# Performance work log

Measured on AMD Instinct MI355X. Metric: run time of the kernel, lower is better.

## Reference

```python
import jax, jax.numpy as jnp
import numpy as np

DIM = 1024
N_HEADS = 16
HEAD_DIM = DIM // N_HEADS
B, T = 4, 2048


def setup_inputs() -> dict:
    key = jax.random.key(0)
    k_x, k_cos, k_sin, k_wqkv, k_wout = jax.random.split(key, 5)
    x = jax.random.normal(k_x, (B, T, DIM), dtype=jnp.float32)
    # rotary tables indexed by position, half the head dim
    pos = jnp.arange(T, dtype=jnp.float32)[:, None]
    inv_freq = 1.0 / (10000.0 ** (jnp.arange(0, HEAD_DIM, 2, dtype=jnp.float32) / HEAD_DIM))
    ang = pos * inv_freq[None, :]  # [T, HEAD_DIM//2]
    cos = jnp.cos(ang)
    sin = jnp.sin(ang)
    mask = jnp.zeros((T, T), dtype=jnp.float32)
    Wqkv = jax.random.normal(k_wqkv, (3 * DIM, DIM), dtype=jnp.float32) * 0.02
    Wout = jax.random.normal(k_wout, (DIM, DIM), dtype=jnp.float32) * 0.02
    return {"x": x, "cos": cos, "sin": sin, "mask": mask, "Wqkv": Wqkv, "Wout": Wout}


def _apply_rope(t, cos, sin):
    # t: [B, T, H, D]; cos/sin: [T, D//2]
    d = t.shape[-1]
    t1, t2 = t[..., : d // 2], t[..., d // 2 :]
    c = cos[: t.shape[1]][None, :, None, :]
    s = sin[: t.shape[1]][None, :, None, :]
    return jnp.concatenate([t1 * c - t2 * s, t1 * s + t2 * c], axis=-1)


def reference(x, cos, sin, mask, Wqkv, Wout):
    Bx, Tx, C = x.shape
    scale = HEAD_DIM ** -0.5
    qkv = (x @ Wqkv.T).reshape(Bx, Tx, 3, N_HEADS, HEAD_DIM)
    q, k, v = qkv[:, :, 0], qkv[:, :, 1], qkv[:, :, 2]
    q = _apply_rope(q, cos, sin)
    k = _apply_rope(k, cos, sin)
    attn = jnp.einsum("bthd,bshd->bhts", q, k) * scale  # [B, H, T, T]
    attn = attn + mask[None, None, :, :]
    p = jax.nn.softmax(attn, axis=-1)
    out = jnp.einsum("bhts,bshd->bthd", p, v).reshape(Bx, Tx, C)
    return out @ Wout.T
```

## Files before the change

### kernel.cpp

```cpp
#include <hip/hip_runtime.h>
#include <math.h>

#define DIMC   1024
#define NHEADS 16
#define HD     64
#define BATCH  4
#define SEQ    2048
#define MROWS  (BATCH * SEQ)
#define QKVC   (3 * DIMC)
#define QSCALE 0.1803368801111204f

typedef __bf16 bf16x8 __attribute__((ext_vector_type(8)));
typedef float  f32x4  __attribute__((ext_vector_type(4)));
typedef short  s16x4  __attribute__((ext_vector_type(4)));
typedef unsigned short us;

#define MFMA16(a, b, c) __builtin_amdgcn_mfma_f32_16x16x32_bf16(a, b, c, 0, 0, 0)

__device__ __forceinline__ f32x4 mfma16x16x16(s16x4 a, s16x4 b, f32x4 c) {
#if __has_builtin(__builtin_amdgcn_mfma_f32_16x16x16bf16_1k)
    return __builtin_amdgcn_mfma_f32_16x16x16bf16_1k(a, b, c, 0, 0, 0);
#else
    asm volatile("v_mfma_f32_16x16x16_bf16 %0, %1, %2, %0"
                 : "+v"(c) : "v"(a), "v"(b));
    return c;
#endif
}

__device__ __forceinline__ void async16(const void* g, void* l) {
    __builtin_amdgcn_global_load_lds(
        (const __attribute__((address_space(1))) void*)g,
        (__attribute__((address_space(3))) void*)l, 16, 0, 0);
}

__device__ __forceinline__ bf16x8 ldsfrag(const us* p) {
    union { int4 q; bf16x8 v; } u;
    u.q = *(const int4*)p;
    return u.v;
}

__device__ __forceinline__ s16x4 ldsfrag64(const us* p) {
    union { uint2 q; s16x4 v; } u;
    u.q = *(const uint2*)p;
    return u.v;
}

__device__ __forceinline__ bf16x8 gfrag(const us* __restrict__ p) {
    union { int4 q; bf16x8 v; } u;
    u.q = *(const int4*)p;
    return u.v;
}

__device__ __forceinline__ us bf16_rn(float f) {
    unsigned int u = __builtin_bit_cast(unsigned int, f);
    u += 0x7fffu + ((u >> 16) & 1u);
    return (us)(u >> 16);
}

__device__ __forceinline__ float fast_exp2(float x) {
#if __has_builtin(__builtin_amdgcn_exp2f)
    return __builtin_amdgcn_exp2f(x);
#else
    return __expf(x * 0.6931471805599453f);
#endif
}

__device__ __forceinline__ s16x4 pack4t(float a, float b, float c, float d) {
    union { unsigned u[2]; s16x4 v; } z;
    z.u[0] = __builtin_amdgcn_perm(__builtin_bit_cast(unsigned, b),
                                   __builtin_bit_cast(unsigned, a), 0x07060302);
    z.u[1] = __builtin_amdgcn_perm(__builtin_bit_cast(unsigned, d),
                                   __builtin_bit_cast(unsigned, c), 0x07060302);
    return z.v;
}

#define NX (MROWS * DIMC)
#define NW (QKVC * DIMC)
#define NO (DIMC * DIMC)
#define NC (SEQ * 32)
__global__ __launch_bounds__(256) void cast3_bf16(const float* __restrict__ x,
                                                  const float* __restrict__ wq,
                                                  const float* __restrict__ wo,
                                                  const float* __restrict__ cosb,
                                                  const float* __restrict__ sinb,
                                                  us* __restrict__ xb,
                                                  us* __restrict__ wqb,
                                                  us* __restrict__ wob,
                                                  float* __restrict__ cs2) {
    int i = (blockIdx.x * 256 + threadIdx.x) * 4;
    const float* src;
    us* dst;
    if (i < NX)                { src = x  + i;             dst = xb  + i; }
    else if (i < NX + NW)      { src = wq + (i - NX);      dst = wqb + (i - NX); }
    else if (i < NX + NW + NO) { src = wo + (i - NX - NW); dst = wob + (i - NX - NW); }
    else {
        int p0 = i - (NX + NW + NO);
        if (p0 >= NC) return;
        float4 c4 = *(const float4*)(cosb + p0);
        float4 s4 = *(const float4*)(sinb + p0);
        float4 o0 = {c4.x, s4.x, c4.y, s4.y};
        float4 o1 = {c4.z, s4.z, c4.w, s4.w};
        *(float4*)(cs2 + 2 * p0)     = o0;
        *(float4*)(cs2 + 2 * p0 + 4) = o1;
        return;
    }
    float4 v = *(const float4*)src;
    ushort4 o = {bf16_rn(v.x), bf16_rn(v.y), bf16_rn(v.z), bf16_rn(v.w)};
    *(ushort4*)dst = o;
}

template <int MODE, int NCOLS, int NBLK>
__global__ __launch_bounds__(512, 2) void gemm256(const us* __restrict__ A,
                                                  const us* __restrict__ B,
                                                  void* __restrict__ Cv,
                                                  const float* __restrict__ cs2,
                                                  us* __restrict__ vt) {
    __shared__ __align__(16) us As[3][256 * 64];
    __shared__ __align__(16) us Bs[3][128 * 64];

    const int tid  = threadIdx.x;
    const int lane = tid & 63, w = tid >> 6;
    const int col  = lane & 15, quad = lane >> 4;
    const int r8   = lane >> 3, c8 = lane & 7;
    const int wm   = (w >> 1) * 64, wn = (w & 1) * 64;

    const int f    = blockIdx.y * gridDim.x + blockIdx.x;
    const int xcd  = f & 7, idx = f >> 3;
    const int m0   = (xcd * 4 + idx / NBLK) * 256;
    const int n0   = (idx % NBLK) * 128;

    const us* Ag = A + (size_t)(m0 + w * 8 + r8) * 1024 + (c8 ^ r8) * 8;
    const us* Bg = B + (size_t)(n0 + w * 8 + r8) * 1024 + (c8 ^ r8) * 8;
    us* Ad = &As[0][0] + w * 512 + lane * 8;
    us* Bd = &Bs[0][0] + w * 512 + lane * 8;

    auto stage = [&](int kt, int bb) __attribute__((always_inline)) {
        const us* ag = Ag + kt * 64;
        us* ad = Ad + bb * (256 * 64);
#pragma unroll
        for (int i = 0; i < 4; ++i)
            async16(ag + (size_t)i * 64 * 1024, ad + i * 4096);
        const us* bg = Bg + kt * 64;
        us* bd = Bd + bb * (128 * 64);
#pragma unroll
        for (int i = 0; i < 2; ++i)
            async16(bg + (size_t)i * 64 * 1024, bd + i * 4096);
    };

    f32x4 acc[4][4] = {};

    stage(0, 0);
    stage(1, 1);
    asm volatile("s_waitcnt vmcnt(6)" ::: "memory");
    __builtin_amdgcn_s_barrier();
    __builtin_amdgcn_sched_barrier(0);

    const int swz = col & 7;
#pragma unroll
    for (int kt = 0; kt < 16; ++kt) {
        if (kt + 2 < 16) stage(kt + 2, (kt + 2) % 3);
        const us* Ab = &As[kt % 3][0];
        const us* Bb = &Bs[kt % 3][0];
#pragma unroll
        for (int kk = 0; kk < 2; ++kk) {
            bf16x8 af[4], bf[4];
#pragma unroll
            for (int mt = 0; mt < 4; ++mt)
                af[mt] = ldsfrag(Ab + (wm + mt * 16 + col) * 64 +
                                 (((kk * 4 + quad) ^ swz) * 8));
#pragma unroll
            for (int nt = 0; nt < 4; ++nt)
                bf[nt] = ldsfrag(Bb + (wn + nt * 16 + col) * 64 +
                                 (((kk * 4 + quad) ^ swz) * 8));
            __builtin_amdgcn_s_setprio(1);
#pragma unroll
            for (int mt = 0; mt < 4; ++mt)
#pragma unroll
                for (int nt = 0; nt < 4; ++nt)
                    acc[mt][nt] = MFMA16(af[mt], bf[nt], acc[mt][nt]);
            __builtin_amdgcn_s_setprio(0);
        }
        if (kt + 2 < 16)
            asm volatile("s_waitcnt vmcnt(6)" ::: "memory");
        else if (kt + 1 < 16)
            asm volatile("s_waitcnt vmcnt(0)" ::: "memory");
        if (kt + 1 < 16) {
            __builtin_amdgcn_s_barrier();
            __builtin_amdgcn_sched_barrier(0);
        }
    }

    if constexpr (MODE == 1) {
        us* C = (us*)Cv;
        const int gcol0 = n0 + wn;
        const bool is_v = (gcol0 >= 2 * DIMC);
        if (is_v) {
            const int hh   = (gcol0 - 2 * DIMC) >> 6;
            const int bidx = (m0 + wm) >> 11;
            const int tb0  = (m0 + wm) & (SEQ - 1);
#pragma unroll
            for (int mt = 0; mt < 4; ++mt) {
                const int tb = tb0 + mt * 16 + quad * 4;
#pragma unroll
                for (int nt = 0; nt < 4; ++nt) {
                    const int d = nt * 16 + col;
                    ushort4 o = {bf16_rn(acc[mt][nt][0]), bf16_rn(acc[mt][nt][1]),
                                 bf16_rn(acc[mt][nt][2]), bf16_rn(acc[mt][nt][3])};
                    *(ushort4*)(vt + ((size_t)((bidx * 16 + hh) * 64 + d)) * SEQ + tb) = o;
                }
            }
        } else {
            const float fq = (gcol0 < DIMC) ? QSCALE : 1.0f;
#pragma unroll
            for (int mt = 0; mt < 4; ++mt) {
#pragma unroll
                for (int r = 0; r < 4; ++r) {
                    const int grow = m0 + wm + mt * 16 + quad * 4 + r;
                    const int t = grow & (SEQ - 1);
#pragma unroll
                    for (int nt = 0; nt < 2; ++nt) {
                        const int d1 = nt * 16 + col;
                        const float2 cs = ((const float2*)cs2)[t * 32 + d1];
                        const float v1 = acc[mt][nt][r];
                        const float v2 = acc[mt][nt + 2][r];
                        C[(size_t)grow * NCOLS + gcol0 + d1]      = bf16_rn((v1 * cs.x - v2 * cs.y) * fq);
                        C[(size_t)grow * NCOLS + gcol0 + d1 + 32] = bf16_rn((v1 * cs.y + v2 * cs.x) * fq);
                    }
                }
            }
        }
    } else {
        float* C = (float*)Cv;
#pragma unroll
        for (int mt = 0; mt < 4; ++mt)
#pragma unroll
            for (int nt = 0; nt < 4; ++nt)
#pragma unroll
                for (int r = 0; r < 4; ++r)
                    C[(size_t)(m0 + wm + mt * 16 + quad * 4 + r) * NCOLS +
                      n0 + wn + nt * 16 + col] = acc[mt][nt][r];
    }
}

__global__ __launch_bounds__(256, 2) void attn_mfma(const us* __restrict__ qkv,
                                                    const us* __restrict__ vt,
                                                    us* __restrict__ outb) {
    __shared__ __align__(16) us Ks[2 * 64 * 64];
    __shared__ __align__(16) us Vs[2 * 64 * 64];

    const int tid  = threadIdx.x;
    const int lane = tid & 63, w = tid >> 6;
    const int col  = lane & 15, quad = lane >> 4;

    const int f  = blockIdx.y * gridDim.x + blockIdx.x;
    const int c  = (f & 7) * 64 + (f >> 3);
    const int bh = c >> 3, b = bh >> 4, h = bh & 15;
    const int t0 = (c & 7) * 256;

    const int r8 = lane >> 3;
    const int cs = ((lane & 7) ^ r8) * 8;

    const int sw0 = ((quad ^ (col & 7)) << 3);
    const int sw4 = sw0 ^ 32;
    const int e2 = quad >> 1, o4 = (quad & 1) * 4, cm = col & 7;

    const us* qb = qkv + (size_t)b * SEQ * QKVC + h * HD;

    bf16x8 aq[4][2];
#pragma unroll
    for (int s = 0; s < 4; ++s)
#pragma unroll
        for (int hf = 0; hf < 2; ++hf)
            aq[s][hf] = gfrag(qb + (size_t)(t0 + s * 64 + w * 16 + col) * QKVC +
                              hf * 32 + quad * 8);

    const us* kg0 = qkv + (size_t)(b * SEQ + w * 16 + r8) * QKVC + DIMC + h * HD + cs;
    const us* vg0 = vt + ((size_t)bh * HD + w * 16 + r8) * SEQ + cs;
    us* kl = Ks + w * 1024 + lane * 8;
    us* vl = Vs + w * 1024 + lane * 8;

    union { us u[4]; s16x4 v; } ones4;
#pragma unroll
    for (int i = 0; i < 4; ++i) ones4.u[i] = 0x3F80;

    f32x4 o_acc[4][4] = {};
    f32x4 lacc[4] = {};

    async16(kg0, kl);
    async16(kg0 + (size_t)8 * QKVC, kl + 512);
    async16(vg0, vl);
    async16(vg0 + (size_t)8 * SEQ, vl + 512);
    asm volatile("s_waitcnt vmcnt(0)" ::: "memory");
    __builtin_amdgcn_s_barrier();
    __builtin_amdgcn_sched_barrier(0);

    int cur = 0;
    for (int s0 = 0; s0 < SEQ; s0 += 64) {
        if (s0 + 64 < SEQ) {
            const int nb = (cur ^ 1) << 12;
            async16(kg0 + (size_t)(s0 + 64) * QKVC, kl + nb);
            async16(kg0 + (size_t)(s0 + 72) * QKVC, kl + nb + 512);
            async16(vg0 + (s0 + 64), vl + nb);
            async16(vg0 + (s0 + 64) + (size_t)8 * SEQ, vl + nb + 512);
        }

        const us* Kb = Ks + (cur << 12);
        const us* Vb = Vs + (cur << 12);

        bf16x8 bk[4][2];
        s16x4  bv[4][4];
#pragma unroll
        for (int nt = 0; nt < 4; ++nt) {
            bk[nt][0] = ldsfrag(Kb + (nt * 16 + col) * 64 + sw0);
            bk[nt][1] = ldsfrag(Kb + (nt * 16 + col) * 64 + sw4);
#pragma unroll
            for (int dt = 0; dt < 4; ++dt)
                bv[nt][dt] = ldsfrag64(Vb + (dt * 16 + col) * 64 +
                                       (((nt * 2 + e2) ^ cm) << 3) + o4);
        }

        f32x4 st[4] = {};
#pragma unroll
        for (int nt = 0; nt < 4; ++nt) {
            st[nt] = MFMA16(bk[nt][0], aq[0][0], st[nt]);
            st[nt] = MFMA16(bk[nt][1], aq[0][1], st[nt]);
        }
#pragma unroll
        for (int s = 0; s < 4; ++s) {
            f32x4 stn[4] = {};
            if (s < 3) {
#pragma unroll
                for (int nt = 0; nt < 4; ++nt) {
                    stn[nt] = MFMA16(bk[nt][0], aq[s + 1][0], stn[nt]);
                    stn[nt] = MFMA16(bk[nt][1], aq[s + 1][1], stn[nt]);
                }
            }
            s16x4 ap[4];
#pragma unroll
            for (int nt = 0; nt < 4; ++nt)
                ap[nt] = pack4t(fast_exp2(st[nt][0]), fast_exp2(st[nt][1]),
                                fast_exp2(st[nt][2]), fast_exp2(st[nt][3]));
#pragma unroll
            for (int nt = 0; nt < 4; ++nt)
                lacc[s] = mfma16x16x16(ap[nt], ones4.v, lacc[s]);
#pragma unroll
            for (int dt = 0; dt < 4; ++dt)
#pragma unroll
                for (int nt = 0; nt < 4; ++nt)
                    o_acc[s][dt] = mfma16x16x16(ap[nt], bv[nt][dt], o_acc[s][dt]);
#pragma unroll
            for (int nt = 0; nt < 4; ++nt) st[nt] = stn[nt];
        }

        asm volatile("s_waitcnt vmcnt(0)" ::: "memory");
        __builtin_amdgcn_s_barrier();
        __builtin_amdgcn_sched_barrier(0);
        cur ^= 1;
    }

#pragma unroll
    for (int s = 0; s < 4; ++s) {
        float linv[4];
#pragma unroll
        for (int r = 0; r < 4; ++r) linv[r] = __builtin_amdgcn_rcpf(lacc[s][r]);
#pragma unroll
        for (int dt = 0; dt < 4; ++dt)
#pragma unroll
            for (int r = 0; r < 4; ++r) {
                const int t = t0 + s * 64 + w * 16 + quad * 4 + r;
                const int d = h * HD + dt * 16 + col;
                outb[(size_t)(b * SEQ + t) * DIMC + d] = bf16_rn(o_acc[s][dt][r] * linv[r]);
            }
    }
}

extern "C" void kernel_launch(void* const* d_in, const int* in_sizes, int n_in,
                              void* d_out, int out_size, void* d_ws, size_t ws_size,
                              hipStream_t stream) {
    const float* x    = (const float*)d_in[0];
    const float* cosb = (const float*)d_in[1];
    const float* sinb = (const float*)d_in[2];
    const float* Wqkv = (const float*)d_in[4];
    const float* Wout = (const float*)d_in[5];
    float* out = (float*)d_out;

    us* xb    = (us*)d_ws;
    us* wqkb  = xb + (size_t)MROWS * DIMC;
    us* woutb = wqkb + (size_t)QKVC * DIMC;
    us* qkvb  = woutb + (size_t)DIMC * DIMC;
    us* vtb   = qkvb + (size_t)MROWS * QKVC;
    us* aob   = vtb + (size_t)BATCH * NHEADS * HD * SEQ;
    float* cs2 = (float*)(aob + (size_t)MROWS * DIMC);

    cast3_bf16<<<(NX + NW + NO + NC) / 1024, 256, 0, stream>>>(
        x, Wqkv, Wout, cosb, sinb, xb, wqkb, woutb, cs2);

    gemm256<1, QKVC, QKVC / 128><<<dim3(QKVC / 128, MROWS / 256), 512, 0, stream>>>(
        xb, wqkb, qkvb, cs2, vtb);

    attn_mfma<<<dim3(SEQ / 256, BATCH * NHEADS), 256, 0, stream>>>(qkvb, vtb, aob);

    gemm256<0, DIMC, DIMC / 128><<<dim3(DIMC / 128, MROWS / 256), 512, 0, stream>>>(
        aob, woutb, out, nullptr, nullptr);
}
```

Baseline: 287.0 us.

## Interleave async tile loads with MFMA phases in the GEMM main loop

After: 289.2 us. About the same (+0.8%).

```diff
diff --git a/kernel.cpp b/kernel.cpp
--- a/kernel.cpp
+++ b/kernel.cpp
@@ -110,7 +110,7 @@
 }
 
 template <int MODE, int NCOLS, int NBLK>
-__global__ __launch_bounds__(512, 2) void gemm256(const us* __restrict__ A,
+__global__ __launch_bounds__(512, 1) void gemm256(const us* __restrict__ A,
                                                   const us* __restrict__ B,
                                                   void* __restrict__ Cv,
                                                   const float* __restrict__ cs2,
@@ -134,23 +134,25 @@
     us* Ad = &As[0][0] + w * 512 + lane * 8;
     us* Bd = &Bs[0][0] + w * 512 + lane * 8;
 
-    auto stage = [&](int kt, int bb) __attribute__((always_inline)) {
+    auto stage0 = [&](int kt, int bb) __attribute__((always_inline)) {
         const us* ag = Ag + kt * 64;
         us* ad = Ad + bb * (256 * 64);
-#pragma unroll
-        for (int i = 0; i < 4; ++i)
-            async16(ag + (size_t)i * 64 * 1024, ad + i * 4096);
-        const us* bg = Bg + kt * 64;
-        us* bd = Bd + bb * (128 * 64);
-#pragma unroll
-        for (int i = 0; i < 2; ++i)
-            async16(bg + (size_t)i * 64 * 1024, bd + i * 4096);
+        async16(ag, ad);
+        async16(ag + (size_t)64 * 1024, ad + 4096);
+        async16(Bg + kt * 64, Bd + bb * (128 * 64));
     };
+    auto stage1 = [&](int kt, int bb) __attribute__((always_inline)) {
+        const us* ag = Ag + kt * 64;
+        us* ad = Ad + bb * (256 * 64);
+        async16(ag + (size_t)128 * 1024, ad + 8192);
+        async16(ag + (size_t)192 * 1024, ad + 12288);
+        async16(Bg + kt * 64 + (size_t)64 * 1024, Bd + bb * (128 * 64) + 4096);
+    };
 
     f32x4 acc[4][4] = {};
 
-    stage(0, 0);
-    stage(1, 1);
+    stage0(0, 0); stage1(0, 0);
+    stage0(1, 1); stage1(1, 1);
     asm volatile("s_waitcnt vmcnt(6)" ::: "memory");
     __builtin_amdgcn_s_barrier();
     __builtin_amdgcn_sched_barrier(0);
@@ -158,20 +160,23 @@
     const int swz = col & 7;
 #pragma unroll
     for (int kt = 0; kt < 16; ++kt) {
-        if (kt + 2 < 16) stage(kt + 2, (kt + 2) % 3);
         const us* Ab = &As[kt % 3][0];
         const us* Bb = &Bs[kt % 3][0];
-#pragma unroll
-        for (int kk = 0; kk < 2; ++kk) {
+        const int nb = (kt + 2) % 3;
+        const bool pf = (kt + 2 < 16);
+
+        {
             bf16x8 af[4], bf[4];
 #pragma unroll
             for (int mt = 0; mt < 4; ++mt)
-                af[mt] = ldsfrag(Ab + (wm + mt * 16 + col) * 64 +
-                                 (((kk * 4 + quad) ^ swz) * 8));
+                af[mt] = ldsfrag(Ab + (wm + mt * 16 + col) * 64 + ((quad ^ swz) * 8));
 #pragma unroll
             for (int nt = 0; nt < 4; ++nt)
-                bf[nt] = ldsfrag(Bb + (wn + nt * 16 + col) * 64 +
-                                 (((kk * 4 + quad) ^ swz) * 8));
+                bf[nt] = ldsfrag(Bb + (wn + nt * 16 + col) * 64 + ((quad ^ swz) * 8));
+            if (pf) stage0(kt + 2, nb);
+            __builtin_amdgcn_s_barrier();
+            asm volatile("s_waitcnt lgkmcnt(0)" ::: "memory");
+            __builtin_amdgcn_sched_barrier(0);
             __builtin_amdgcn_s_setprio(1);
 #pragma unroll
             for (int mt = 0; mt < 4; ++mt)
@@ -179,12 +184,31 @@
                 for (int nt = 0; nt < 4; ++nt)
                     acc[mt][nt] = MFMA16(af[mt], bf[nt], acc[mt][nt]);
             __builtin_amdgcn_s_setprio(0);
-        }
-        if (kt + 2 < 16)
-            asm volatile("s_waitcnt vmcnt(6)" ::: "memory");
-        else if (kt + 1 < 16)
-            asm volatile("s_waitcnt vmcnt(0)" ::: "memory");
-        if (kt + 1 < 16) {
+            __builtin_amdgcn_s_barrier();
+        }
+        {
+            bf16x8 af[4], bf[4];
+#pragma unroll
+            for (int mt = 0; mt < 4; ++mt)
+                af[mt] = ldsfrag(Ab + (wm + mt * 16 + col) * 64 + (((4 + quad) ^ swz) * 8));
+#pragma unroll
+            for (int nt = 0; nt < 4; ++nt)
+                bf[nt] = ldsfrag(Bb + (wn + nt * 16 + col) * 64 + (((4 + quad) ^ swz) * 8));
+            if (pf) stage1(kt + 2, nb);
+            __builtin_amdgcn_s_barrier();
+            asm volatile("s_waitcnt lgkmcnt(0)" ::: "memory");
+            __builtin_amdgcn_sched_barrier(0);
+            __builtin_amdgcn_s_setprio(1);
+#pragma unroll
+            for (int mt = 0; mt < 4; ++mt)
+#pragma unroll
+                for (int nt = 0; nt < 4; ++nt)
+                    acc[mt][nt] = MFMA16(af[mt], bf[nt], acc[mt][nt]);
+            __builtin_amdgcn_s_setprio(0);
+            if (kt + 2 < 16)
+                asm volatile("s_waitcnt vmcnt(6)" ::: "memory");
+            else if (kt + 1 < 16)
+                asm volatile("s_waitcnt vmcnt(0)" ::: "memory");
             __builtin_amdgcn_s_barrier();
             __builtin_amdgcn_sched_barrier(0);
         }
```
